# Optimization experiments

Measured on AMD Instinct MI355X. Metric: run time of the kernel, lower is better.

The kernel has to match this reference:

```python
import jax, jax.numpy as jnp
import numpy as np

N_HEAD = 16
HEAD_DIM = 64
N_EMBD = N_HEAD * HEAD_DIM  # 1024


def setup_inputs() -> dict:
    key = jax.random.key(0)
    ks = jax.random.split(key, 5)
    B, S = 2, 2048
    x = jax.random.normal(ks[0], (B, S, N_EMBD), dtype=jnp.float32)
    qkv_w = jax.random.normal(ks[1], (N_EMBD, 3 * N_EMBD), dtype=jnp.float32) * 0.02
    qkv_b = jax.random.normal(ks[2], (3 * N_EMBD,), dtype=jnp.float32) * 0.02
    proj_w = jax.random.normal(ks[3], (N_EMBD, N_EMBD), dtype=jnp.float32) * 0.02
    proj_b = jax.random.normal(ks[4], (N_EMBD,), dtype=jnp.float32) * 0.02
    return {"x": x, "qkv_w": qkv_w, "qkv_b": qkv_b, "proj_w": proj_w, "proj_b": proj_b}


def reference(x, qkv_w, qkv_b, proj_w, proj_b):
    B, S, _ = x.shape
    qkv = x @ qkv_w + qkv_b  # [B,S,3E]
    q, k, v = jnp.split(qkv, 3, axis=-1)
    # [B,H,S,D]
    q = q.reshape(B, S, N_HEAD, HEAD_DIM).transpose(0, 2, 1, 3)
    k = k.reshape(B, S, N_HEAD, HEAD_DIM).transpose(0, 2, 1, 3)
    v = v.reshape(B, S, N_HEAD, HEAD_DIM).transpose(0, 2, 1, 3)
    scale = 1.0 / jnp.sqrt(jnp.float32(HEAD_DIM))
    scores = jnp.einsum('bhqd,bhkd->bhqk', q, k) * scale  # [B,H,S,S]
    causal = jnp.tril(jnp.ones((S, S), dtype=bool))
    scores = jnp.where(causal[None, None], scores, jnp.float32(-jnp.inf))
    attn = jax.nn.softmax(scores, axis=-1)  # dropout p=0 (eval)
    out = jnp.einsum('bhqk,bhkd->bhqd', attn, v)
    out = out.transpose(0, 2, 1, 3).reshape(B, S, N_EMBD)
    out = out @ proj_w + proj_b  # resid dropout p=0
    return out, k, v
```

## Files before the change

kernel.cpp:

```cpp
#include <hip/hip_runtime.h>
#include <hip/hip_bf16.h>


typedef __attribute__((ext_vector_type(4))) float f32x4;
typedef __attribute__((ext_vector_type(16))) float f32x16;
typedef __attribute__((ext_vector_type(8))) short s16x8;
typedef __attribute__((ext_vector_type(4))) short s16x4;

__device__ __forceinline__ short f2bf(float f) {
    union { float f; unsigned u; } x{f};
    unsigned r = x.u + 0x7fff + ((x.u >> 16) & 1);
    return (short)(r >> 16);
}

__device__ __forceinline__ void gload_lds16(const void* g, void* l) {
    __builtin_amdgcn_global_load_lds(
        (const __attribute__((address_space(1))) void*)g,
        (__attribute__((address_space(3))) void*)l, 16, 0, 0);
}

__global__ __launch_bounds__(256) void fused_prepass(const float* __restrict__ x,
                                                     short* __restrict__ x_bf,
                                                     const float* __restrict__ qkv_w,
                                                     short* __restrict__ wT1,
                                                     const float* __restrict__ proj_w,
                                                     short* __restrict__ wT2) {
    __shared__ float tile[32][33];
    const int bid = blockIdx.x, tid = threadIdx.x;
    if (bid < 2048) {
        int i = (bid * 256 + tid) * 8;
        f32x4 a = *(const f32x4*)&x[i];
        f32x4 b = *(const f32x4*)&x[i + 4];
        s16x8 o;
        #pragma unroll
        for (int j = 0; j < 4; ++j) o[j] = f2bf(a[j]);
        #pragma unroll
        for (int j = 0; j < 4; ++j) o[j + 4] = f2bf(b[j]);
        *(s16x8*)&x_bf[i] = o;
        return;
    }
    const float* in;
    short* out;
    int K = 1024, N, n0, k0;
    if (bid < 5120) {
        int blk = bid - 2048;
        in = qkv_w; out = wT1; N = 3072;
        n0 = (blk % 96) * 32; k0 = (blk / 96) * 32;
    } else {
        int blk = bid - 5120;
        in = proj_w; out = wT2; N = 1024;
        n0 = (blk & 31) * 32; k0 = (blk >> 5) * 32;
    }
    const int tx = tid & 31, ty = tid >> 5;
    #pragma unroll
    for (int r = 0; r < 4; ++r)
        tile[ty + r * 8][tx] = in[(long)(k0 + ty + r * 8) * N + n0 + tx];
    __syncthreads();
    #pragma unroll
    for (int r = 0; r < 4; ++r)
        out[(long)(n0 + ty + r * 8) * K + k0 + tx] = f2bf(tile[tx][ty + r * 8]);
}

template <int MODE>
__global__ __launch_bounds__(512, 4) void gemm_bf16(
    const short* __restrict__ A, const short* __restrict__ Bt,
    const float* __restrict__ bias, int M, int N, int K,
    float* __restrict__ outf,
    short* __restrict__ qbf, short* __restrict__ kbf, short* __restrict__ vbfT,
    float* __restrict__ kout, float* __restrict__ vout) {
    __shared__ __align__(16) short As[2][128 * 64];
    __shared__ __align__(16) short Bs[2][128 * 64];
    const int tid = threadIdx.x;
    const int l = tid & 63, wv = tid >> 6;
    const int grp = wv >> 2, w = wv & 3;
    const int lr = l >> 4, lc = l & 15;
    const int wm = w >> 1, wn = w & 1;
    const int bid = blockIdx.x;
    const int xcd = bid & 7, s = bid >> 3;
    int bx, by;
    if (MODE == 1) { bx = (xcd & 1) * 12 + s % 12; by = (xcd >> 1) * 8 + s / 12; }
    else           { bx = (xcd & 1) * 4 + (s & 3); by = (xcd >> 1) * 8 + (s >> 2); }
    const int m0 = by * 128, n0 = bx * 128;
    const int gtid = tid & 255;

    f32x4 acc[4][4] = {};

    for (int it = 0; it < 8; ++it) {
        const int kb = grp * 512 + it * 64;
        __syncthreads();
        #pragma unroll
        for (int j = 0; j < 4; ++j) {
            const int c = gtid + 256 * j;
            const int row = c >> 3;
            const int lseg = (c & 7) ^ (row & 7);
            gload_lds16(A + (long)(m0 + row) * K + kb + lseg * 8, &As[grp][c * 8]);
            gload_lds16(Bt + (long)(n0 + row) * K + kb + lseg * 8, &Bs[grp][c * 8]);
        }
        __syncthreads();
        #pragma unroll
        for (int kh = 0; kh < 2; ++kh) {
            s16x8 af[4], bfr[4];
            #pragma unroll
            for (int mi = 0; mi < 4; ++mi) {
                const int row = wm * 64 + mi * 16 + lc;
                af[mi] = *(const s16x8*)&As[grp][row * 64 + (((kh * 4 + lr) ^ (lc & 7)) * 8)];
            }
            #pragma unroll
            for (int ni = 0; ni < 4; ++ni) {
                const int row = wn * 64 + ni * 16 + lc;
                bfr[ni] = *(const s16x8*)&Bs[grp][row * 64 + (((kh * 4 + lr) ^ (lc & 7)) * 8)];
            }
            #pragma unroll
            for (int mi = 0; mi < 4; ++mi)
                #pragma unroll
                for (int ni = 0; ni < 4; ++ni)
                    acc[mi][ni] = __builtin_amdgcn_mfma_f32_16x16x32_bf16(
                        af[mi], bfr[ni], acc[mi][ni], 0, 0, 0);
        }
    }

    __syncthreads();
    float* MB = (float*)&As[0][0];
    float* reg = (w < 2) ? (float*)&As[w][0] : (float*)&Bs[w - 2][0];
    if (grp == 1) {
        #pragma unroll
        for (int mi = 0; mi < 4; ++mi)
            #pragma unroll
            for (int ni = 0; ni < 4; ++ni)
                #pragma unroll
                for (int i = 0; i < 4; ++i)
                    reg[(mi * 16 + lr * 4 + i) * 64 + ni * 16 + lc] = acc[mi][ni][i];
    }
    __syncthreads();
    if (grp == 1) return;
    #pragma unroll
    for (int mi = 0; mi < 4; ++mi)
        #pragma unroll
        for (int ni = 0; ni < 4; ++ni)
            #pragma unroll
            for (int i = 0; i < 4; ++i)
                acc[mi][ni][i] += reg[(mi * 16 + lr * 4 + i) * 64 + ni * 16 + lc];
    (void)MB;

    #pragma unroll
    for (int mi = 0; mi < 4; ++mi) {
        #pragma unroll
        for (int ni = 0; ni < 4; ++ni) {
            int col = n0 + wn * 64 + ni * 16 + lc;
            float bv = bias[col];
            if (MODE == 1) {
                int sec = col >> 10, rem = col & 1023;
                int h = rem >> 6, d = rem & 63;
                int row0 = m0 + wm * 64 + mi * 16 + lr * 4;
                int b = row0 >> 11, s0 = row0 & 2047;
                long idxSD = ((long)((b << 4) + h) * 2048 + s0) * 64 + d;
                if (sec == 0) {
                    #pragma unroll
                    for (int i = 0; i < 4; ++i) {
                        float val = acc[mi][ni][i] + bv;
                        qbf[idxSD + (long)i * 64] = f2bf(val * 0.1803368801111244f);
                    }
                } else if (sec == 1) {
                    #pragma unroll
                    for (int i = 0; i < 4; ++i) {
                        float val = acc[mi][ni][i] + bv;
                        kout[idxSD + (long)i * 64] = val;
                        kbf[idxSD + (long)i * 64] = f2bf(val);
                    }
                } else {
                    s16x4 pk;
                    #pragma unroll
                    for (int i = 0; i < 4; ++i) {
                        float val = acc[mi][ni][i] + bv;
                        vout[idxSD + (long)i * 64] = val;
                        pk[i] = f2bf(val);
                    }
                    *(s16x4*)&vbfT[((long)((b << 4) + h) * 64 + d) * 2048 + s0] = pk;
                }
            } else {
                #pragma unroll
                for (int i = 0; i < 4; ++i) {
                    int row = m0 + wm * 64 + mi * 16 + lr * 4 + i;
                    outf[(long)row * N + col] = acc[mi][ni][i] + bv;
                }
            }
        }
    }
}

__global__ __launch_bounds__(512, 4) void attn_kernel(const short* __restrict__ qbf,
                                                      const short* __restrict__ kbf,
                                                      const short* __restrict__ vbfT,
                                                      short* __restrict__ obf) {
    const int bid = blockIdx.x;
    const int xcd = bid & 7, r = bid >> 3;
    const int head_local = r & 3, q16 = r >> 2;
    const int qt = (q16 < 8) ? (q16 + 8) : (15 - q16);
    const int bh = xcd * 4 + head_local;
    const int tid = threadIdx.x;
    const int wv = tid >> 6, l = tid & 63;
    const int strip = wv & 3, kh = wv >> 2;
    const int h = l >> 5;
    const int l8 = l & 7;
    const int q0 = qt * 128 + strip * 32;
    const int qlane = q0 + (l & 31);
    const long baseSD = (long)bh * 2048 * 64;
    const long baseDS = (long)bh * 64 * 2048;

    __shared__ __align__(16) short Ks[2][64 * 64];
    __shared__ __align__(16) short Vs[2][64 * 64];
    __shared__ __align__(16) float MG[4][64][36];

    const int sSub = l >> 3;
    const int sChunk = (l & 7) ^ sSub;
    auto stage = [&](int kt, int nb) {
        const int k0 = kt * 64;
        const int r0 = wv * 8 + sSub;
        gload_lds16(kbf + baseSD + (long)(k0 + r0) * 64 + sChunk * 8,
                    &Ks[nb][(wv * 8) * 64]);
        gload_lds16(vbfT + baseDS + (long)r0 * 2048 + k0 + sChunk * 8,
                    &Vs[nb][(wv * 8) * 64]);
    };

    s16x8 qf[4];
    #pragma unroll
    for (int dd = 0; dd < 4; ++dd)
        qf[dd] = *(const s16x8*)&qbf[baseSD + (long)qlane * 64 + dd * 16 + h * 8];

    f32x4 lacc = {};
    f32x16 O[2] = {};

    const int nkt = 2 * qt + 2;

    stage(0, 0);
    __syncthreads();
    int cur = 0;

    for (int kt = 0; kt < nkt; ++kt) {
        if (kt + 1 < nkt) stage(kt + 1, cur ^ 1);
        const int kbase = kt * 64 + kh * 32;

        if (kbase <= q0 + 31) {
            const short* Kb = Ks[cur];
            const short* Vb = Vs[cur];
            f32x16 z = {};
            #pragma unroll
            for (int dd = 0; dd < 4; ++dd) {
                s16x8 kf = *(const s16x8*)&Kb[(kh * 32 + (l & 31)) * 64 +
                                              (((2 * dd + h) ^ l8) * 8)];
                z = __builtin_amdgcn_mfma_f32_32x32x16_bf16(kf, qf[dd], z, 0, 0, 0);
            }
            if (kbase + 31 > q0) {
                #pragma unroll
                for (int rr = 0; rr < 16; ++rr) {
                    int kpos = kbase + (rr & 3) + 8 * (rr >> 2) + 4 * h;
                    if (kpos > qlane) z[rr] = -INFINITY;
                }
            }
            float p[16];
            #pragma unroll
            for (int rr = 0; rr < 16; ++rr) {
                p[rr] = __builtin_amdgcn_exp2f(z[rr]);
                lacc[rr & 3] += p[rr];
            }
            #pragma unroll
            for (int f = 0; f < 2; ++f) {
                union { __hip_bfloat162 b2[4]; s16x8 v; } pk;
                #pragma unroll
                for (int j = 0; j < 4; ++j)
                    pk.b2[j] = __float22bfloat162_rn(
                        make_float2(p[f * 8 + 2 * j], p[f * 8 + 2 * j + 1]));
                const int c0 = kh * 4 + f * 2;
                #pragma unroll
                for (int dt2 = 0; dt2 < 2; ++dt2) {
                    const short* vr = &Vb[(dt2 * 32 + (l & 31)) * 64];
                    s16x8 vf;
                    *(s16x4*)&vf = *(const s16x4*)&vr[(c0 ^ l8) * 8 + 4 * h];
                    *(((s16x4*)&vf) + 1) = *(const s16x4*)&vr[((c0 + 1) ^ l8) * 8 + 4 * h];
                    O[dt2] = __builtin_amdgcn_mfma_f32_32x32x16_bf16(vf, pk.v,
                                                                     O[dt2], 0, 0, 0);
                }
            }
        }
        __syncthreads();
        cur ^= 1;
    }

    float lsum = (lacc[0] + lacc[1]) + (lacc[2] + lacc[3]);
    if (kh == 1) {
        float* row = &MG[strip][l][0];
        #pragma unroll
        for (int dt2 = 0; dt2 < 2; ++dt2)
            #pragma unroll
            for (int rr = 0; rr < 16; ++rr)
                row[dt2 * 16 + rr] = O[dt2][rr];
        row[32] = lsum;
    }
    __syncthreads();
    if (kh == 0) {
        const float* row = &MG[strip][l][0];
        lsum += row[32];
        lsum += __shfl_xor(lsum, 32);
        const int b = bh >> 4, hd = bh & 15;
        float inv = 1.0f / lsum;
        #pragma unroll
        for (int dt2 = 0; dt2 < 2; ++dt2) {
            #pragma unroll
            for (int g = 0; g < 4; ++g) {
                s16x4 o;
                #pragma unroll
                for (int i = 0; i < 4; ++i)
                    o[i] = f2bf((O[dt2][g * 4 + i] + row[dt2 * 16 + g * 4 + i]) * inv);
                const int d = dt2 * 32 + 8 * g + 4 * h;
                *(s16x4*)&obf[(long)(b * 2048 + qlane) * 1024 + hd * 64 + d] = o;
            }
        }
    }
}


extern "C" void kernel_launch(void* const* d_in, const int* in_sizes, int n_in,
                              void* d_out, int out_size, void* d_ws, size_t ws_size,
                              hipStream_t stream) {
    const float* x = (const float*)d_in[0];
    const float* qkv_w = (const float*)d_in[1];
    const float* qkv_b = (const float*)d_in[2];
    const float* proj_w = (const float*)d_in[3];
    const float* proj_b = (const float*)d_in[4];

    float* out = (float*)d_out;
    float* kout = out + 4194304;
    float* vout = out + 8388608;

    short* x_bf = (short*)d_ws;
    short* wT1 = x_bf + 4194304;
    short* wT2 = wT1 + 3145728;
    short* q_bf = wT2 + 1048576;
    short* k_bf = q_bf + 4194304;
    short* vT_bf = k_bf + 4194304;
    short* o_bf = x_bf;

    fused_prepass<<<6144, 256, 0, stream>>>(x, x_bf, qkv_w, wT1, proj_w, wT2);

    gemm_bf16<1><<<768, 512, 0, stream>>>(x_bf, wT1, qkv_b, 4096, 3072, 1024,
                                          nullptr, q_bf, k_bf, vT_bf, kout, vout);

    attn_kernel<<<512, 512, 0, stream>>>(q_bf, k_bf, vT_bf, o_bf);

    gemm_bf16<2><<<256, 512, 0, stream>>>(o_bf, wT2, proj_b, 4096, 1024, 1024,
                                          out, nullptr, nullptr, nullptr, nullptr, nullptr);
}
```

Baseline: 111.0 us.

## Drop split-K in QKV GEMM, use 256-thread blocks with full-K loop

```diff
diff --git a/kernel.cpp b/kernel.cpp
--- a/kernel.cpp
+++ b/kernel.cpp
@@ -61,13 +61,99 @@
         out[(long)(n0 + ty + r * 8) * K + k0 + tx] = f2bf(tile[tx][ty + r * 8]);
 }
 
-template <int MODE>
-__global__ __launch_bounds__(512, 4) void gemm_bf16(
+__global__ __launch_bounds__(256) void gemm1_bf16(
     const short* __restrict__ A, const short* __restrict__ Bt,
     const float* __restrict__ bias, int M, int N, int K,
-    float* __restrict__ outf,
     short* __restrict__ qbf, short* __restrict__ kbf, short* __restrict__ vbfT,
     float* __restrict__ kout, float* __restrict__ vout) {
+    __shared__ __align__(16) short As[128 * 64];
+    __shared__ __align__(16) short Bs[128 * 64];
+    const int tid = threadIdx.x;
+    const int l = tid & 63, w = tid >> 6;
+    const int lr = l >> 4, lc = l & 15;
+    const int wm = w >> 1, wn = w & 1;
+    const int bid = blockIdx.x;
+    const int xcd = bid & 7, s = bid >> 3;
+    const int bx = (xcd & 1) * 12 + s % 12, by = (xcd >> 1) * 8 + s / 12;
+    const int m0 = by * 128, n0 = bx * 128;
+
+    f32x4 acc[4][4] = {};
+
+    for (int kb = 0; kb < K; kb += 64) {
+        __syncthreads();
+        #pragma unroll
+        for (int j = 0; j < 4; ++j) {
+            const int c = tid + 256 * j;
+            const int row = c >> 3;
+            const int lseg = (c & 7) ^ (row & 7);
+            gload_lds16(A + (long)(m0 + row) * K + kb + lseg * 8, As + c * 8);
+            gload_lds16(Bt + (long)(n0 + row) * K + kb + lseg * 8, Bs + c * 8);
+        }
+        __syncthreads();
+        #pragma unroll
+        for (int kh = 0; kh < 2; ++kh) {
+            s16x8 af[4], bfr[4];
+            #pragma unroll
+            for (int mi = 0; mi < 4; ++mi) {
+                const int row = wm * 64 + mi * 16 + lc;
+                af[mi] = *(const s16x8*)&As[row * 64 + (((kh * 4 + lr) ^ (lc & 7)) * 8)];
+            }
+            #pragma unroll
+            for (int ni = 0; ni < 4; ++ni) {
+                const int row = wn * 64 + ni * 16 + lc;
+                bfr[ni] = *(const s16x8*)&Bs[row * 64 + (((kh * 4 + lr) ^ (lc & 7)) * 8)];
+            }
+            #pragma unroll
+            for (int mi = 0; mi < 4; ++mi)
+                #pragma unroll
+                for (int ni = 0; ni < 4; ++ni)
+                    acc[mi][ni] = __builtin_amdgcn_mfma_f32_16x16x32_bf16(
+                        af[mi], bfr[ni], acc[mi][ni], 0, 0, 0);
+        }
+    }
+
+    #pragma unroll
+    for (int mi = 0; mi < 4; ++mi) {
+        #pragma unroll
+        for (int ni = 0; ni < 4; ++ni) {
+            int col = n0 + wn * 64 + ni * 16 + lc;
+            float bv = bias[col];
+            int sec = col >> 10, rem = col & 1023;
+            int h = rem >> 6, d = rem & 63;
+            int row0 = m0 + wm * 64 + mi * 16 + lr * 4;
+            int b = row0 >> 11, s0 = row0 & 2047;
+            long idxSD = ((long)((b << 4) + h) * 2048 + s0) * 64 + d;
+            if (sec == 0) {
+                #pragma unroll
+                for (int i = 0; i < 4; ++i) {
+                    float val = acc[mi][ni][i] + bv;
+                    qbf[idxSD + (long)i * 64] = f2bf(val * 0.1803368801111244f);
+                }
+            } else if (sec == 1) {
+                #pragma unroll
+                for (int i = 0; i < 4; ++i) {
+                    float val = acc[mi][ni][i] + bv;
+                    kout[idxSD + (long)i * 64] = val;
+                    kbf[idxSD + (long)i * 64] = f2bf(val);
+                }
+            } else {
+                s16x4 pk;
+                #pragma unroll
+                for (int i = 0; i < 4; ++i) {
+                    float val = acc[mi][ni][i] + bv;
+                    vout[idxSD + (long)i * 64] = val;
+                    pk[i] = f2bf(val);
+                }
+                *(s16x4*)&vbfT[((long)((b << 4) + h) * 64 + d) * 2048 + s0] = pk;
+            }
+        }
+    }
+}
+
+__global__ __launch_bounds__(512) void gemm2_bf16(
+    const short* __restrict__ A, const short* __restrict__ Bt,
+    const float* __restrict__ bias, int M, int N, int K,
+    float* __restrict__ outf) {
     __shared__ __align__(16) short As[2][128 * 64];
     __shared__ __align__(16) short Bs[2][128 * 64];
     const int tid = threadIdx.x;
@@ -77,9 +163,7 @@
     const int wm = w >> 1, wn = w & 1;
     const int bid = blockIdx.x;
     const int xcd = bid & 7, s = bid >> 3;
-    int bx, by;
-    if (MODE == 1) { bx = (xcd & 1) * 12 + s % 12; by = (xcd >> 1) * 8 + s / 12; }
-    else           { bx = (xcd & 1) * 4 + (s & 3); by = (xcd >> 1) * 8 + (s >> 2); }
+    const int bx = (xcd & 1) * 4 + (s & 3), by = (xcd >> 1) * 8 + (s >> 2);
     const int m0 = by * 128, n0 = bx * 128;
     const int gtid = tid & 255;
 
@@ -120,7 +204,6 @@
     }
 
     __syncthreads();
-    float* MB = (float*)&As[0][0];
     float* reg = (w < 2) ? (float*)&As[w][0] : (float*)&Bs[w - 2][0];
     if (grp == 1) {
         #pragma unroll
@@ -140,7 +223,6 @@
             #pragma unroll
             for (int i = 0; i < 4; ++i)
                 acc[mi][ni][i] += reg[(mi * 16 + lr * 4 + i) * 64 + ni * 16 + lc];
-    (void)MB;
 
     #pragma unroll
     for (int mi = 0; mi < 4; ++mi) {
@@ -148,41 +230,10 @@
         for (int ni = 0; ni < 4; ++ni) {
             int col = n0 + wn * 64 + ni * 16 + lc;
             float bv = bias[col];
-            if (MODE == 1) {
-                int sec = col >> 10, rem = col & 1023;
-                int h = rem >> 6, d = rem & 63;
-                int row0 = m0 + wm * 64 + mi * 16 + lr * 4;
-                int b = row0 >> 11, s0 = row0 & 2047;
-                long idxSD = ((long)((b << 4) + h) * 2048 + s0) * 64 + d;
-                if (sec == 0) {
-                    #pragma unroll
-                    for (int i = 0; i < 4; ++i) {
-                        float val = acc[mi][ni][i] + bv;
-                        qbf[idxSD + (long)i * 64] = f2bf(val * 0.1803368801111244f);
-                    }
-                } else if (sec == 1) {
-                    #pragma unroll
-                    for (int i = 0; i < 4; ++i) {
-                        float val = acc[mi][ni][i] + bv;
-                        kout[idxSD + (long)i * 64] = val;
-                        kbf[idxSD + (long)i * 64] = f2bf(val);
-                    }
-                } else {
-                    s16x4 pk;
-                    #pragma unroll
-                    for (int i = 0; i < 4; ++i) {
-                        float val = acc[mi][ni][i] + bv;
-                        vout[idxSD + (long)i * 64] = val;
-                        pk[i] = f2bf(val);
-                    }
-                    *(s16x4*)&vbfT[((long)((b << 4) + h) * 64 + d) * 2048 + s0] = pk;
-                }
-            } else {
-                #pragma unroll
-                for (int i = 0; i < 4; ++i) {
-                    int row = m0 + wm * 64 + mi * 16 + lr * 4 + i;
-                    outf[(long)row * N + col] = acc[mi][ni][i] + bv;
-                }
+            #pragma unroll
+            for (int i = 0; i < 4; ++i) {
+                int row = m0 + wm * 64 + mi * 16 + lr * 4 + i;
+                outf[(long)row * N + col] = acc[mi][ni][i] + bv;
             }
         }
     }
@@ -342,11 +393,10 @@
 
     fused_prepass<<<6144, 256, 0, stream>>>(x, x_bf, qkv_w, wT1, proj_w, wT2);
 
-    gemm_bf16<1><<<768, 512, 0, stream>>>(x_bf, wT1, qkv_b, 4096, 3072, 1024,
-                                          nullptr, q_bf, k_bf, vT_bf, kout, vout);
+    gemm1_bf16<<<768, 256, 0, stream>>>(x_bf, wT1, qkv_b, 4096, 3072, 1024,
+                                        q_bf, k_bf, vT_bf, kout, vout);
 
     attn_kernel<<<512, 512, 0, stream>>>(q_bf, k_bf, vT_bf, o_bf);
 
-    gemm_bf16<2><<<256, 512, 0, stream>>>(o_bf, wT2, proj_b, 4096, 1024, 1024,
-                                          out, nullptr, nullptr, nullptr, nullptr, nullptr);
-}
+    gemm2_bf16<<<256, 512, 0, stream>>>(o_bf, wT2, proj_b, 4096, 1024, 1024, out);
+}
```

Result: faster. 99.69 us (median of 2 runs) (-10.2%).
